# Optimization experiments

Hardware: AMD Instinct MI355X
Metric: run time of the kernel (lower is better)

The kernel has to match this reference:

```python
import jax, jax.numpy as jnp
import numpy as np

DIM = 192
NUM_HEADS = 6
WS = (7, 7, 7)
N_TOK = WS[0] * WS[1] * WS[2]  # 343
TABLE_SIZE = (2 * WS[0] - 1) * (2 * WS[1] - 1) * (2 * WS[2] - 1)  # 2197


def _relative_position_index():
    # faithful replication of the torch buffer construction (incl. its strides)
    coords = np.stack(np.meshgrid(np.arange(WS[0]), np.arange(WS[1]), np.arange(WS[2]), indexing='ij'))
    flat = coords.reshape(3, -1)                     # [3, N]
    rel = flat[:, :, None] - flat[:, None, :]        # [3, N, N]
    rel = rel.transpose(1, 2, 0).astype(np.int64)    # [N, N, 3]
    rel[..., 0] += WS[0] - 1
    rel[..., 1] += WS[1] - 1
    rel[..., 2] += WS[2] - 1
    rel[..., 0] *= 3 * WS[1] - 1  # = 20 (source uses window_size[1] here)
    rel[..., 1] *= 2 * WS[1] - 1  # = 13
    return rel.sum(-1)            # [N, N]


def setup_inputs() -> dict:
    key = jax.random.key(0)
    ks = jax.random.split(key, 10)
    B_, nW = 256, 64
    x1 = jax.random.normal(ks[0], (B_, N_TOK, DIM), dtype=jnp.float32)
    x2 = jax.random.normal(ks[1], (B_, N_TOK, DIM), dtype=jnp.float32)
    mask = jax.random.normal(ks[2], (nW, N_TOK, N_TOK), dtype=jnp.float32)
    table = 0.02 * jax.random.normal(ks[3], (TABLE_SIZE, NUM_HEADS), dtype=jnp.float32)
    s = DIM ** -0.5
    q_w = s * jax.random.normal(ks[4], (DIM, DIM), dtype=jnp.float32)
    q_b = jnp.zeros((DIM,), jnp.float32)
    kv_w = s * jax.random.normal(ks[5], (2 * DIM, DIM), dtype=jnp.float32)
    kv_b = jnp.zeros((2 * DIM,), jnp.float32)
    proj_w = s * jax.random.normal(ks[6], (DIM, DIM), dtype=jnp.float32)
    proj_b = jnp.zeros((DIM,), jnp.float32)
    rel_idx = jnp.asarray(_relative_position_index(), dtype=jnp.int32)
    return {"x1": x1, "x2": x2, "mask": mask, "table": table,
            "q_w": q_w, "q_b": q_b, "kv_w": kv_w, "kv_b": kv_b,
            "proj_w": proj_w, "proj_b": proj_b, "rel_idx": rel_idx}


def reference(x1, x2, mask, table, q_w, q_b, kv_w, kv_b, proj_w, proj_b, rel_idx):
    B_, N, C = x1.shape
    H = NUM_HEADS
    hd = C // H
    scale = hd ** -0.5
    # q from x1, k/v from x2 (isfusion cross-attention path)
    q = (x1 @ q_w.T + q_b).reshape(B_, N, H, hd).transpose(0, 2, 1, 3) * scale  # [B,H,N,hd]
    kv = (x2 @ kv_w.T + kv_b).reshape(B_, N, 2, H, hd).transpose(2, 0, 3, 1, 4)  # [2,B,H,N,hd]
    k, v = kv[0], kv[1]
    attn = jnp.einsum('bhnd,bhmd->bhnm', q, k)  # [B,H,N,N]
    # relative position bias gather -> [H,N,N]
    bias = table[rel_idx.reshape(-1)].reshape(N, N, H).transpose(2, 0, 1)
    attn = attn + bias[None]
    # shifted-window mask add
    nW = mask.shape[0]
    attn = (attn.reshape(B_ // nW, nW, H, N, N) + mask[None, :, None]).reshape(B_, H, N, N)
    attn = jax.nn.softmax(attn, axis=-1)
    out = jnp.einsum('bhnm,bhmd->bnhd', attn, v).reshape(B_, N, C)
    return out @ proj_w.T + proj_b
```

## Files before the change

### kernel.cpp

```cpp
#include <hip/hip_runtime.h>

typedef __attribute__((ext_vector_type(8))) short short8;
typedef __attribute__((ext_vector_type(4))) float f32x4;
typedef __attribute__((ext_vector_type(16))) float f32x16;
typedef __attribute__((ext_vector_type(4))) unsigned short us4;
typedef __attribute__((ext_vector_type(2))) unsigned int u32x2;

#define NTOK 343
#define BMP 352
#define LOG2E 1.4426950408889634f
#define FPLANE 11264
#define WPITCH 200

#define OFF_QG   0u
#define OFF_KG   33718272u
#define OFF_VT   68321280u
#define OFF_AO   102924288u
#define OFF_WB   136642560u

__device__ __forceinline__ unsigned short f2bf(float f) {
  union { float f; unsigned u; } v; v.f = f;
  unsigned r = v.u + 0x7FFFu + ((v.u >> 16) & 1u);
  return (unsigned short)(r >> 16);
}

__device__ __forceinline__ float bf2f(unsigned short b) {
  union { unsigned u; float f; } v; v.u = ((unsigned)b) << 16;
  return v.f;
}

__device__ __forceinline__ short8 ld8(const unsigned short* p) {
  return *reinterpret_cast<const short8*>(p);
}

__device__ __forceinline__ float fexp2(float x) {
  float r; asm("v_exp_f32 %0, %1" : "=v"(r) : "v"(x)); return r;
}

__device__ __forceinline__ unsigned cvtpk(float a, float b) {
  unsigned r; asm("v_cvt_pk_bf16_f32 %0, %1, %2" : "=v"(r) : "v"(a), "v"(b)); return r;
}

__device__ __forceinline__ f32x16 mfma32(short8 a, short8 b, f32x16 c) {
  return __builtin_amdgcn_mfma_f32_32x32x16_bf16(a, b, c, 0, 0, 0);
}

__device__ __forceinline__ f32x4 mfma16(short8 a, short8 b, f32x4 c) {
  return __builtin_amdgcn_mfma_f32_16x16x32_bf16(a, b, c, 0, 0, 0);
}

union frag_u { unsigned u[4]; short8 s8; };

__global__ __launch_bounds__(256) void precompute(
    const float* __restrict__ x1, const float* __restrict__ x2,
    const float* __restrict__ mask, const float* __restrict__ table,
    const int* __restrict__ rel_idx,
    const float* __restrict__ qw, const float* __restrict__ kvw, const float* __restrict__ pw,
    unsigned short* __restrict__ x1b, unsigned short* __restrict__ x2b,
    unsigned short* __restrict__ wq_bf, unsigned short* __restrict__ wkv_bf,
    unsigned short* __restrict__ wp_bf,
    unsigned short* __restrict__ bias_bf, unsigned short* __restrict__ mask_bf,
    unsigned short* __restrict__ v_frag)
{
  const int idx = blockIdx.x * 256 + threadIdx.x;
  if (idx < 8429568) {
    const float* src; unsigned short* dst; int i;
    if (idx < 4214784) { src = x1; dst = x1b; i = idx; }
    else               { src = x2; dst = x2b; i = idx - 4214784; }
    f32x4 v = *reinterpret_cast<const f32x4*>(src + i * 4);
    us4 o; o[0] = f2bf(v[0]); o[1] = f2bf(v[1]); o[2] = f2bf(v[2]); o[3] = f2bf(v[3]);
    *reinterpret_cast<us4*>(dst + i * 4) = o;
  } else if (idx < 8466432) {
    const int wi = idx - 8429568;
    const float* src; unsigned short* dst; int i;
    if (wi < 9216)       { src = qw;  dst = wq_bf;  i = wi; }
    else if (wi < 27648) { src = kvw; dst = wkv_bf; i = wi - 9216; }
    else                 { src = pw;  dst = wp_bf;  i = wi - 27648; }
    f32x4 v = *reinterpret_cast<const f32x4*>(src + i * 4);
    us4 o; o[0] = f2bf(v[0]); o[1] = f2bf(v[1]); o[2] = f2bf(v[2]); o[3] = f2bf(v[3]);
    *reinterpret_cast<us4*>(dst + i * 4) = o;
  } else if (idx < 10398208) {
    const int mi = idx - 8466432;
    const int row = mi / 88, q = mi - row * 88;
    const int j0 = q * 4;
    unsigned short* dst = mask_bf + row * BMP + j0;
    if (q < 85) {
      const float* src = mask + row * NTOK + j0;
      us4 o; o[0] = f2bf(LOG2E * src[0]); o[1] = f2bf(LOG2E * src[1]);
      o[2] = f2bf(LOG2E * src[2]); o[3] = f2bf(LOG2E * src[3]);
      *reinterpret_cast<us4*>(dst) = o;
    } else {
      us4 o;
      #pragma unroll
      for (int i = 0; i < 4; ++i) {
        const int col = j0 + i;
        o[i] = (col < NTOK) ? f2bf(LOG2E * mask[row * NTOK + col]) : (unsigned short)0;
      }
      *reinterpret_cast<us4*>(dst) = o;
    }
  } else if (idx < 10515857) {
    const int i = idx - 10398208;
    const int ri = rel_idx[i] * 6;
    const int rrow = i / NTOK, j = i - rrow * NTOK;
    unsigned short* dst = bias_bf + rrow * BMP + j;
    #pragma unroll
    for (int h = 0; h < 6; ++h) dst[h * (NTOK * BMP)] = f2bf(LOG2E * table[ri + h]);
  } else if (idx < 10517915) {
    const int p = idx - 10515857;
    unsigned short* dst = bias_bf + p * BMP + NTOK;
    #pragma unroll
    for (int c = 0; c < 9; ++c) dst[c] = 0;
  } else if (idx < 10714523) {
    const int i = idx - 10517915;
    const int bh = i >> 7, c = i & 127;
    short8 z = (short8){0,0,0,0,0,0,0,0};
    *reinterpret_cast<short8*>(v_frag + bh * FPLANE + 10240 + c * 8) = z;
  }
}

__global__ __launch_bounds__(256) void proj(
    const unsigned short* __restrict__ x1b, const unsigned short* __restrict__ x2b,
    const unsigned short* __restrict__ wq_bf, const unsigned short* __restrict__ wkv_bf,
    const float* __restrict__ qb, const float* __restrict__ kvb,
    unsigned short* __restrict__ q_g, unsigned short* __restrict__ k_g,
    unsigned short* __restrict__ v_frag)
{
  __shared__ __align__(16) unsigned short wLds[192 * WPITCH];

  const int tid = threadIdx.x;
  const int wv = tid >> 6, lane = tid & 63, lg = lane >> 4, lr = lane & 15;
  const int path = blockIdx.y;
  const int b = blockIdx.x & 255, seg = blockIdx.x >> 8;
  const int n0 = seg * 128 + wv * 32;

  const unsigned short* X = (path == 0) ? x1b : x2b;
  const unsigned short* Wsrc = (path == 0) ? wq_bf : (path == 1 ? wkv_bf : wkv_bf + 36864);

  #pragma unroll
  for (int i = 0; i < 18; ++i) {
    const int c = i * 256 + tid;
    const int row = c / 24, c8 = c - row * 24;
    *reinterpret_cast<short8*>(&wLds[row * WPITCH + c8 * 8]) = ld8(Wsrc + row * 192 + c8 * 8);
  }
  __syncthreads();

  const int rowbase = b * NTOK;
  const int nA = n0 + lr, nB = n0 + 16 + lr;
  const unsigned short* xr0 = X + (rowbase + (nA < NTOK ? nA : NTOK - 1)) * 192 + lg * 8;
  const unsigned short* xr1 = X + (rowbase + (nB < NTOK ? nB : NTOK - 1)) * 192 + lg * 8;

  short8 ax[2][6];
  #pragma unroll
  for (int kk = 0; kk < 6; ++kk) {
    ax[0][kk] = ld8(xr0 + kk * 32);
    ax[1][kk] = ld8(xr1 + kk * 32);
  }

  f32x4 acc[2][12];
  #pragma unroll
  for (int i = 0; i < 2; ++i)
    #pragma unroll
    for (int j = 0; j < 12; ++j) acc[i][j] = (f32x4){0.f, 0.f, 0.f, 0.f};

  if (path < 2) {
    #pragma unroll
    for (int kk = 0; kk < 6; ++kk) {
      const int k0 = kk * 32 + lg * 8;
      #pragma unroll
      for (int ct = 0; ct < 12; ++ct) {
        const short8 wf = *reinterpret_cast<const short8*>(&wLds[(ct * 16 + lr) * WPITCH + k0]);
        acc[0][ct] = mfma16(wf, ax[0][kk], acc[0][ct]);
        acc[1][ct] = mfma16(wf, ax[1][kk], acc[1][ct]);
      }
    }
    if (path == 0) {
      const float qs = 0.17677669529663687f * LOG2E;
      #pragma unroll
      for (int tt = 0; tt < 2; ++tt) {
        const int n = n0 + tt * 16 + lr;
        if (n < NTOK) {
          unsigned short* ob = q_g + (b * 6 * NTOK + n) * 32 + (lg & 1) * 0;
          #pragma unroll
          for (int ct = 0; ct < 12; ++ct) {
            const f32x4 bb = *reinterpret_cast<const f32x4*>(qb + ct * 16 + lg * 4);
            u32x2 pk;
            pk[0] = cvtpk((acc[tt][ct][0] + bb[0]) * qs, (acc[tt][ct][1] + bb[1]) * qs);
            pk[1] = cvtpk((acc[tt][ct][2] + bb[2]) * qs, (acc[tt][ct][3] + bb[3]) * qs);
            *reinterpret_cast<u32x2*>(ob + (ct >> 1) * (NTOK * 32) + (ct & 1) * 16 + lg * 4) = pk;
          }
        }
      }
    } else {
      #pragma unroll
      for (int tt = 0; tt < 2; ++tt) {
        const int n = n0 + tt * 16 + lr;
        if (n < 352) {
          unsigned short* ob = k_g + b * 6 * FPLANE + (n >> 5) * 1024
                               + ((lg >> 1) * 32 + (n & 31)) * 8 + (lg & 1) * 4;
          #pragma unroll
          for (int ct = 0; ct < 12; ++ct) {
            const f32x4 bb = *reinterpret_cast<const f32x4*>(kvb + ct * 16 + lg * 4);
            u32x2 pk;
            pk[0] = cvtpk(acc[tt][ct][0] + bb[0], acc[tt][ct][1] + bb[1]);
            pk[1] = cvtpk(acc[tt][ct][2] + bb[2], acc[tt][ct][3] + bb[3]);
            *reinterpret_cast<u32x2*>(ob + (ct >> 1) * FPLANE + (ct & 1) * 512) = pk;
          }
        }
      }
    }
  } else {
    #pragma unroll
    for (int kk = 0; kk < 6; ++kk) {
      const int k0 = kk * 32 + lg * 8;
      #pragma unroll
      for (int ct = 0; ct < 12; ++ct) {
        const short8 wf = *reinterpret_cast<const short8*>(&wLds[(ct * 16 + lr) * WPITCH + k0]);
        acc[0][ct] = mfma16(ax[0][kk], wf, acc[0][ct]);
        acc[1][ct] = mfma16(ax[1][kk], wf, acc[1][ct]);
      }
    }
    float bs[12];
    #pragma unroll
    for (int ct = 0; ct < 12; ++ct) bs[ct] = kvb[192 + ct * 16 + lr];
    const int d2lo = lr;
    #pragma unroll
    for (int tt = 0; tt < 2; ++tt) {
      const int nb = n0 + tt * 16 + lg * 4;
      if (nb < 352) {
        unsigned short* vb = v_frag + b * 6 * FPLANE + (nb >> 5) * 1024
                             + ((nb >> 4) & 1) * 512 + ((nb >> 3) & 1) * 256 + (nb & 7);
        #pragma unroll
        for (int ct = 0; ct < 12; ++ct) {
          const int d = (ct & 1) * 16 + d2lo;
          u32x2 pk;
          pk[0] = cvtpk(acc[tt][ct][0] + bs[ct], acc[tt][ct][1] + bs[ct]);
          pk[1] = cvtpk(acc[tt][ct][2] + bs[ct], acc[tt][ct][3] + bs[ct]);
          *reinterpret_cast<u32x2*>(vb + (ct >> 1) * FPLANE + d * 8) = pk;
        }
      }
    }
  }
}

__global__ __launch_bounds__(256, 3) void attn(
    const unsigned short* __restrict__ q_g, const unsigned short* __restrict__ k_g,
    const unsigned short* __restrict__ v_frag, const unsigned short* __restrict__ bias_bf,
    const unsigned short* __restrict__ mask_bf, unsigned short* __restrict__ attn_out)
{
  __shared__ __align__(16) unsigned short kvlds[2][FPLANE];

  const int tid = threadIdx.x;
  const int wv = tid >> 6, lane = tid & 63;
  const int l31 = lane & 31, hi = lane >> 5;
  const int bid = blockIdx.x;
  const int b = bid / 6, h = bid - b * 6;
  const int w = b & 63;

  const unsigned short* qp = q_g + bid * (NTOK * 32);
  const unsigned short* kpf = k_g + bid * FPLANE;
  const unsigned short* vpf = v_frag + bid * FPLANE;
  const unsigned short* bias_h = bias_bf + h * (NTOK * BMP);
  const unsigned short* mask_w = mask_bf + w * (NTOK * BMP);

  #pragma unroll
  for (int j = 0; j < 6; ++j) {
    const int c = j * 256 + tid;
    if (c < 1408) {
      *reinterpret_cast<short8*>(&kvlds[0][c * 8]) = ld8(kpf + c * 8);
      *reinterpret_cast<short8*>(&kvlds[1][c * 8]) = ld8(vpf + c * 8);
    }
  }
  __syncthreads();

  for (int qt = wv; qt < 11; qt += 4) {
    const int qq = qt * 32 + l31;
    const int qrc = qq < NTOK ? qq : NTOK - 1;
    const short8 qf0 = ld8(qp + qrc * 32 + hi * 8);
    const short8 qf1 = ld8(qp + qrc * 32 + 16 + hi * 8);
    const unsigned short* bmb = bias_h + qrc * BMP + hi * 4;
    const unsigned short* bmm = mask_w + qrc * BMP + hi * 4;

    f32x16 O;
    #pragma unroll
    for (int r = 0; r < 16; ++r) O[r] = 0.f;
    float m = -3.0e38f, sum = 0.f;

    us4 nb[4], nm[4];
    #pragma unroll
    for (int g = 0; g < 4; ++g) {
      nb[g] = *reinterpret_cast<const us4*>(bmb + g * 8);
      nm[g] = *reinterpret_cast<const us4*>(bmm + g * 8);
    }

    #pragma unroll
    for (int kt = 0; kt < 11; ++kt) {
      us4 cb[4], cm[4];
      #pragma unroll
      for (int g = 0; g < 4; ++g) { cb[g] = nb[g]; cm[g] = nm[g]; }
      if (kt < 10) {
        const int kn = (kt + 1) * 32;
        #pragma unroll
        for (int g = 0; g < 4; ++g) {
          nb[g] = *reinterpret_cast<const us4*>(bmb + kn + g * 8);
          nm[g] = *reinterpret_cast<const us4*>(bmm + kn + g * 8);
        }
      }

      const short8 kf0 = ld8(&kvlds[0][kt * 1024 + lane * 8]);
      const short8 kf1 = ld8(&kvlds[0][kt * 1024 + 512 + lane * 8]);
      f32x16 s;
      #pragma unroll
      for (int r = 0; r < 16; ++r) s[r] = 0.f;
      s = mfma32(kf0, qf0, s);
      s = mfma32(kf1, qf1, s);

      float p[16];
      float tmax = -3.0e38f;
      #pragma unroll
      for (int g = 0; g < 4; ++g) {
        #pragma unroll
        for (int j = 0; j < 4; ++j) {
          float v = s[g * 4 + j] + (bf2f(cb[g][j]) + bf2f(cm[g][j]));
          if (kt == 10 && (g * 8 + hi * 4 + j) >= 23) v = -3.0e38f;
          p[g * 4 + j] = v;
          tmax = fmaxf(tmax, v);
        }
      }
      tmax = fmaxf(tmax, __shfl_xor(tmax, 32));

      if (!__all(tmax <= m + 8.f)) {
        const float newm = fmaxf(m, tmax);
        const float sc = fexp2(m - newm);
        m = newm;
        sum *= sc;
        #pragma unroll
        for (int r = 0; r < 16; ++r) O[r] *= sc;
      }

      #pragma unroll
      for (int r = 0; r < 16; ++r) p[r] = fexp2(p[r] - m);
      #pragma unroll
      for (int r = 0; r < 16; ++r) sum += p[r];

      const unsigned c01 = cvtpk(p[0], p[1]),  c23 = cvtpk(p[2], p[3]);
      const unsigned c45 = cvtpk(p[4], p[5]),  c67 = cvtpk(p[6], p[7]);
      const unsigned d01 = cvtpk(p[8], p[9]),  d23 = cvtpk(p[10], p[11]);
      const unsigned d45 = cvtpk(p[12], p[13]), d67 = cvtpk(p[14], p[15]);
      const unsigned sc01 = __shfl_xor((int)c01, 32), sc23 = __shfl_xor((int)c23, 32);
      const unsigned sc45 = __shfl_xor((int)c45, 32), sc67 = __shfl_xor((int)c67, 32);
      const unsigned sd01 = __shfl_xor((int)d01, 32), sd23 = __shfl_xor((int)d23, 32);
      const unsigned sd45 = __shfl_xor((int)d45, 32), sd67 = __shfl_xor((int)d67, 32);
      frag_u P0, P1;
      P0.u[0] = hi ? sc45 : c01;  P0.u[1] = hi ? sc67 : c23;
      P0.u[2] = hi ? c45 : sc01;  P0.u[3] = hi ? c67 : sc23;
      P1.u[0] = hi ? sd45 : d01;  P1.u[1] = hi ? sd67 : d23;
      P1.u[2] = hi ? d45 : sd01;  P1.u[3] = hi ? d67 : sd23;

      const short8 vf0 = ld8(&kvlds[1][kt * 1024 + lane * 8]);
      const short8 vf1 = ld8(&kvlds[1][kt * 1024 + 512 + lane * 8]);
      O = mfma32(vf0, P0.s8, O);
      O = mfma32(vf1, P1.s8, O);
    }

    const float sumT = sum + __shfl_xor(sum, 32);
    const float inv = 1.0f / sumT;
    if (qq < NTOK) {
      unsigned short* op = attn_out + (b * NTOK + qq) * 192 + h * 32;
      #pragma unroll
      for (int g = 0; g < 4; ++g) {
        us4 ov;
        #pragma unroll
        for (int j = 0; j < 4; ++j) ov[j] = f2bf(O[g * 4 + j] * inv);
        *reinterpret_cast<us4*>(op + g * 8 + hi * 4) = ov;
      }
    }
  }
}

__global__ __launch_bounds__(256) void proj_out(
    const unsigned short* __restrict__ a_in, const unsigned short* __restrict__ wp_bf,
    const float* __restrict__ pb, float* __restrict__ out)
{
  __shared__ __align__(16) unsigned short wLds[192 * WPITCH];

  const int tid = threadIdx.x;
  const int wv = tid >> 6, lane = tid & 63, lg = lane >> 4, lr = lane & 15;
  const int t0 = blockIdx.x * 128 + wv * 32;

  #pragma unroll
  for (int i = 0; i < 18; ++i) {
    const int c = i * 256 + tid;
    const int row = c / 24, c8 = c - row * 24;
    *reinterpret_cast<short8*>(&wLds[row * WPITCH + c8 * 8]) = ld8(wp_bf + row * 192 + c8 * 8);
  }
  __syncthreads();

  const unsigned short* xr0 = a_in + (t0 + lr) * 192 + lg * 8;
  const unsigned short* xr1 = xr0 + 16 * 192;

  short8 ax[2][6];
  #pragma unroll
  for (int kk = 0; kk < 6; ++kk) {
    ax[0][kk] = ld8(xr0 + kk * 32);
    ax[1][kk] = ld8(xr1 + kk * 32);
  }

  f32x4 acc[2][12];
  #pragma unroll
  for (int i = 0; i < 2; ++i)
    #pragma unroll
    for (int j = 0; j < 12; ++j) acc[i][j] = (f32x4){0.f, 0.f, 0.f, 0.f};

  #pragma unroll
  for (int kk = 0; kk < 6; ++kk) {
    const int k0 = kk * 32 + lg * 8;
    #pragma unroll
    for (int ct = 0; ct < 12; ++ct) {
      const short8 wf = *reinterpret_cast<const short8*>(&wLds[(ct * 16 + lr) * WPITCH + k0]);
      acc[0][ct] = mfma16(wf, ax[0][kk], acc[0][ct]);
      acc[1][ct] = mfma16(wf, ax[1][kk], acc[1][ct]);
    }
  }

  #pragma unroll
  for (int tt = 0; tt < 2; ++tt) {
    const int t = t0 + tt * 16 + lr;
    float* op = out + t * 192 + lg * 4;
    #pragma unroll
    for (int ct = 0; ct < 12; ++ct) {
      const f32x4 bb = *reinterpret_cast<const f32x4*>(pb + ct * 16 + lg * 4);
      f32x4 ov;
      #pragma unroll
      for (int r = 0; r < 4; ++r) ov[r] = acc[tt][ct][r] + bb[r];
      *reinterpret_cast<f32x4*>(op + ct * 16) = ov;
    }
  }
}

extern "C" void kernel_launch(void* const* d_in, const int* in_sizes, int n_in,
                              void* d_out, int out_size, void* d_ws, size_t ws_size,
                              hipStream_t stream) {
  const float* x1    = (const float*)d_in[0];
  const float* x2    = (const float*)d_in[1];
  const float* mask  = (const float*)d_in[2];
  const float* table = (const float*)d_in[3];
  const float* qw    = (const float*)d_in[4];
  const float* qb    = (const float*)d_in[5];
  const float* kvw   = (const float*)d_in[6];
  const float* kvb   = (const float*)d_in[7];
  const float* pw    = (const float*)d_in[8];
  const float* pb    = (const float*)d_in[9];
  const int* rel_idx = (const int*)d_in[10];

  char* ws = (char*)d_ws;
  char* outc = (char*)d_out;
  unsigned short* q_g     = (unsigned short*)(ws + OFF_QG);
  unsigned short* k_g     = (unsigned short*)(ws + OFF_KG);
  unsigned short* v_frag  = (unsigned short*)(ws + OFF_VT);
  unsigned short* a_o     = (unsigned short*)(ws + OFF_AO);
  unsigned short* wq_bf   = (unsigned short*)(ws + OFF_WB);
  unsigned short* wkv_bf  = wq_bf + 36864;
  unsigned short* wp_bf   = wkv_bf + 73728;
  unsigned short* x1b     = a_o;
  unsigned short* x2b     = (unsigned short*)outc;
  unsigned short* bias_bf = (unsigned short*)(outc + 33718272);
  unsigned short* mask_bf = (unsigned short*)(outc + 35167104);

  hipLaunchKernelGGL(precompute, dim3(41854), dim3(256), 0, stream,
                     x1, x2, mask, table, rel_idx, qw, kvw, pw,
                     x1b, x2b, wq_bf, wkv_bf, wp_bf, bias_bf, mask_bf, v_frag);
  hipLaunchKernelGGL(proj, dim3(768, 3), dim3(256), 0, stream,
                     x1b, x2b, wq_bf, wkv_bf, qb, kvb, q_g, k_g, v_frag);
  hipLaunchKernelGGL(attn, dim3(1536), dim3(256), 0, stream,
                     q_g, k_g, v_frag, bias_bf, mask_bf, a_o);
  hipLaunchKernelGGL(proj_out, dim3(686), dim3(256), 0, stream,
                     a_o, wp_bf, pb, (float*)d_out);
}
```

Baseline: 238.1 us.

## Drop online softmax max, use permlane32 swap, remap blocks per XCD, 512 threads

Measured after the change: 368.4 us. 1.55x slower.

```diff
diff --git a/kernel.cpp b/kernel.cpp
--- a/kernel.cpp
+++ b/kernel.cpp
@@ -39,6 +39,10 @@
 
 __device__ __forceinline__ unsigned cvtpk(float a, float b) {
   unsigned r; asm("v_cvt_pk_bf16_f32 %0, %1, %2" : "=v"(r) : "v"(a), "v"(b)); return r;
+}
+
+__device__ __forceinline__ void plswap(unsigned &a, unsigned &b) {
+  asm("v_permlane32_swap_b32 %0, %1" : "+v"(a), "+v"(b));
 }
 
 __device__ __forceinline__ f32x16 mfma32(short8 a, short8 b, f32x16 c) {
@@ -179,7 +183,7 @@
       for (int tt = 0; tt < 2; ++tt) {
         const int n = n0 + tt * 16 + lr;
         if (n < NTOK) {
-          unsigned short* ob = q_g + (b * 6 * NTOK + n) * 32 + (lg & 1) * 0;
+          unsigned short* ob = q_g + (b * 6 * NTOK + n) * 32;
           #pragma unroll
           for (int ct = 0; ct < 12; ++ct) {
             const f32x4 bb = *reinterpret_cast<const f32x4*>(qb + ct * 16 + lg * 4);
@@ -222,7 +226,6 @@
     float bs[12];
     #pragma unroll
     for (int ct = 0; ct < 12; ++ct) bs[ct] = kvb[192 + ct * 16 + lr];
-    const int d2lo = lr;
     #pragma unroll
     for (int tt = 0; tt < 2; ++tt) {
       const int nb = n0 + tt * 16 + lg * 4;
@@ -231,7 +234,7 @@
                              + ((nb >> 4) & 1) * 512 + ((nb >> 3) & 1) * 256 + (nb & 7);
         #pragma unroll
         for (int ct = 0; ct < 12; ++ct) {
-          const int d = (ct & 1) * 16 + d2lo;
+          const int d = (ct & 1) * 16 + lr;
           u32x2 pk;
           pk[0] = cvtpk(acc[tt][ct][0] + bs[ct], acc[tt][ct][1] + bs[ct]);
           pk[1] = cvtpk(acc[tt][ct][2] + bs[ct], acc[tt][ct][3] + bs[ct]);
@@ -242,7 +245,7 @@
   }
 }
 
-__global__ __launch_bounds__(256, 3) void attn(
+__global__ __launch_bounds__(512, 6) void attn(
     const unsigned short* __restrict__ q_g, const unsigned short* __restrict__ k_g,
     const unsigned short* __restrict__ v_frag, const unsigned short* __restrict__ bias_bf,
     const unsigned short* __restrict__ mask_bf, unsigned short* __restrict__ attn_out)
@@ -252,9 +255,12 @@
   const int tid = threadIdx.x;
   const int wv = tid >> 6, lane = tid & 63;
   const int l31 = lane & 31, hi = lane >> 5;
-  const int bid = blockIdx.x;
-  const int b = bid / 6, h = bid - b * 6;
-  const int w = b & 63;
+  const int s0 = blockIdx.x;
+  const int xcd = s0 & 7, ii = s0 >> 3;
+  const int g = xcd * 48 + (ii >> 2), mem = ii & 3;
+  const int h = g >> 6, w = g & 63;
+  const int b = mem * 64 + w;
+  const int bid = b * 6 + h;
 
   const unsigned short* qp = q_g + bid * (NTOK * 32);
   const unsigned short* kpf = k_g + bid * FPLANE;
@@ -263,8 +269,8 @@
   const unsigned short* mask_w = mask_bf + w * (NTOK * BMP);
 
   #pragma unroll
-  for (int j = 0; j < 6; ++j) {
-    const int c = j * 256 + tid;
+  for (int j = 0; j < 3; ++j) {
+    const int c = j * 512 + tid;
     if (c < 1408) {
       *reinterpret_cast<short8*>(&kvlds[0][c * 8]) = ld8(kpf + c * 8);
       *reinterpret_cast<short8*>(&kvlds[1][c * 8]) = ld8(vpf + c * 8);
@@ -272,7 +278,7 @@
   }
   __syncthreads();
 
-  for (int qt = wv; qt < 11; qt += 4) {
+  for (int qt = wv; qt < 11; qt += 8) {
     const int qq = qt * 32 + l31;
     const int qrc = qq < NTOK ? qq : NTOK - 1;
     const short8 qf0 = ld8(qp + qrc * 32 + hi * 8);
@@ -283,78 +289,60 @@
     f32x16 O;
     #pragma unroll
     for (int r = 0; r < 16; ++r) O[r] = 0.f;
-    float m = -3.0e38f, sum = 0.f;
+    f32x4 sacc = (f32x4){0.f, 0.f, 0.f, 0.f};
 
     us4 nb[4], nm[4];
     #pragma unroll
-    for (int g = 0; g < 4; ++g) {
-      nb[g] = *reinterpret_cast<const us4*>(bmb + g * 8);
-      nm[g] = *reinterpret_cast<const us4*>(bmm + g * 8);
+    for (int gg = 0; gg < 4; ++gg) {
+      nb[gg] = *reinterpret_cast<const us4*>(bmb + gg * 8);
+      nm[gg] = *reinterpret_cast<const us4*>(bmm + gg * 8);
     }
 
     #pragma unroll
     for (int kt = 0; kt < 11; ++kt) {
       us4 cb[4], cm[4];
       #pragma unroll
-      for (int g = 0; g < 4; ++g) { cb[g] = nb[g]; cm[g] = nm[g]; }
+      for (int gg = 0; gg < 4; ++gg) { cb[gg] = nb[gg]; cm[gg] = nm[gg]; }
       if (kt < 10) {
         const int kn = (kt + 1) * 32;
         #pragma unroll
-        for (int g = 0; g < 4; ++g) {
-          nb[g] = *reinterpret_cast<const us4*>(bmb + kn + g * 8);
-          nm[g] = *reinterpret_cast<const us4*>(bmm + kn + g * 8);
+        for (int gg = 0; gg < 4; ++gg) {
+          nb[gg] = *reinterpret_cast<const us4*>(bmb + kn + gg * 8);
+          nm[gg] = *reinterpret_cast<const us4*>(bmm + kn + gg * 8);
         }
       }
 
       const short8 kf0 = ld8(&kvlds[0][kt * 1024 + lane * 8]);
       const short8 kf1 = ld8(&kvlds[0][kt * 1024 + 512 + lane * 8]);
-      f32x16 s;
-      #pragma unroll
-      for (int r = 0; r < 16; ++r) s[r] = 0.f;
-      s = mfma32(kf0, qf0, s);
-      s = mfma32(kf1, qf1, s);
+      f32x16 sv;
+      #pragma unroll
+      for (int r = 0; r < 16; ++r) sv[r] = 0.f;
+      sv = mfma32(kf0, qf0, sv);
+      sv = mfma32(kf1, qf1, sv);
 
       float p[16];
-      float tmax = -3.0e38f;
-      #pragma unroll
-      for (int g = 0; g < 4; ++g) {
+      #pragma unroll
+      for (int gg = 0; gg < 4; ++gg) {
         #pragma unroll
         for (int j = 0; j < 4; ++j) {
-          float v = s[g * 4 + j] + (bf2f(cb[g][j]) + bf2f(cm[g][j]));
-          if (kt == 10 && (g * 8 + hi * 4 + j) >= 23) v = -3.0e38f;
-          p[g * 4 + j] = v;
-          tmax = fmaxf(tmax, v);
+          float v = sv[gg * 4 + j] + (bf2f(cb[gg][j]) + bf2f(cm[gg][j]));
+          if (kt == 10 && (gg * 8 + hi * 4 + j) >= 23) v = -3.0e38f;
+          p[gg * 4 + j] = fexp2(v);
         }
       }
-      tmax = fmaxf(tmax, __shfl_xor(tmax, 32));
-
-      if (!__all(tmax <= m + 8.f)) {
-        const float newm = fmaxf(m, tmax);
-        const float sc = fexp2(m - newm);
-        m = newm;
-        sum *= sc;
-        #pragma unroll
-        for (int r = 0; r < 16; ++r) O[r] *= sc;
-      }
-
-      #pragma unroll
-      for (int r = 0; r < 16; ++r) p[r] = fexp2(p[r] - m);
-      #pragma unroll
-      for (int r = 0; r < 16; ++r) sum += p[r];
-
-      const unsigned c01 = cvtpk(p[0], p[1]),  c23 = cvtpk(p[2], p[3]);
-      const unsigned c45 = cvtpk(p[4], p[5]),  c67 = cvtpk(p[6], p[7]);
-      const unsigned d01 = cvtpk(p[8], p[9]),  d23 = cvtpk(p[10], p[11]);
-      const unsigned d45 = cvtpk(p[12], p[13]), d67 = cvtpk(p[14], p[15]);
-      const unsigned sc01 = __shfl_xor((int)c01, 32), sc23 = __shfl_xor((int)c23, 32);
-      const unsigned sc45 = __shfl_xor((int)c45, 32), sc67 = __shfl_xor((int)c67, 32);
-      const unsigned sd01 = __shfl_xor((int)d01, 32), sd23 = __shfl_xor((int)d23, 32);
-      const unsigned sd45 = __shfl_xor((int)d45, 32), sd67 = __shfl_xor((int)d67, 32);
+      #pragma unroll
+      for (int j = 0; j < 4; ++j)
+        sacc[j] += (p[j] + p[4 + j]) + (p[8 + j] + p[12 + j]);
+
+      unsigned c01 = cvtpk(p[0], p[1]),   c23 = cvtpk(p[2], p[3]);
+      unsigned c45 = cvtpk(p[4], p[5]),   c67 = cvtpk(p[6], p[7]);
+      unsigned d01 = cvtpk(p[8], p[9]),   d23 = cvtpk(p[10], p[11]);
+      unsigned d45 = cvtpk(p[12], p[13]), d67 = cvtpk(p[14], p[15]);
+      plswap(c01, c45); plswap(c23, c67);
+      plswap(d01, d45); plswap(d23, d67);
       frag_u P0, P1;
-      P0.u[0] = hi ? sc45 : c01;  P0.u[1] = hi ? sc67 : c23;
-      P0.u[2] = hi ? c45 : sc01;  P0.u[3] = hi ? c67 : sc23;
-      P1.u[0] = hi ? sd45 : d01;  P1.u[1] = hi ? sd67 : d23;
-      P1.u[2] = hi ? d45 : sd01;  P1.u[3] = hi ? d67 : sd23;
+      P0.u[0] = c01; P0.u[1] = c23; P0.u[2] = c45; P0.u[3] = c67;
+      P1.u[0] = d01; P1.u[1] = d23; P1.u[2] = d45; P1.u[3] = d67;
 
       const short8 vf0 = ld8(&kvlds[1][kt * 1024 + lane * 8]);
       const short8 vf1 = ld8(&kvlds[1][kt * 1024 + 512 + lane * 8]);
@@ -362,16 +350,17 @@
       O = mfma32(vf1, P1.s8, O);
     }
 
-    const float sumT = sum + __shfl_xor(sum, 32);
-    const float inv = 1.0f / sumT;
+    float sum = (sacc[0] + sacc[1]) + (sacc[2] + sacc[3]);
+    sum += __shfl_xor(sum, 32);
+    const float inv = 1.0f / sum;
     if (qq < NTOK) {
       unsigned short* op = attn_out + (b * NTOK + qq) * 192 + h * 32;
       #pragma unroll
-      for (int g = 0; g < 4; ++g) {
+      for (int gg = 0; gg < 4; ++gg) {
         us4 ov;
         #pragma unroll
-        for (int j = 0; j < 4; ++j) ov[j] = f2bf(O[g * 4 + j] * inv);
-        *reinterpret_cast<us4*>(op + g * 8 + hi * 4) = ov;
+        for (int j = 0; j < 4; ++j) ov[j] = f2bf(O[gg * 4 + j] * inv);
+        *reinterpret_cast<us4*>(op + gg * 8 + hi * 4) = ov;
       }
     }
   }
@@ -471,7 +460,7 @@
                      x1b, x2b, wq_bf, wkv_bf, wp_bf, bias_bf, mask_bf, v_frag);
   hipLaunchKernelGGL(proj, dim3(768, 3), dim3(256), 0, stream,
                      x1b, x2b, wq_bf, wkv_bf, qb, kvb, q_g, k_g, v_frag);
-  hipLaunchKernelGGL(attn, dim3(1536), dim3(256), 0, stream,
+  hipLaunchKernelGGL(attn, dim3(1536), dim3(512), 0, stream,
                      q_g, k_g, v_frag, bias_bf, mask_bf, a_o);
   hipLaunchKernelGGL(proj_out, dim3(686), dim3(256), 0, stream,
                      a_o, wp_bf, pb, (float*)d_out);
```
